# Kernel tuning notes

Hardware: AMD Instinct MI355X
Metric: run time of the kernel (lower is better)

Reference implementation:

```python
import jax, jax.numpy as jnp
import numpy as np
import math

B, T, C, H = 2, 2048, 768, 12
HD = C // H
EPS = 1e-5

def setup_inputs() -> dict:
    key = jax.random.key(0)
    ks = jax.random.split(key, 12)
    s = lambda n: 1.0 / math.sqrt(n)
    return {
        "x": jax.random.normal(ks[0], (B, T, C), jnp.float32),
        "ln1_g": jnp.ones((C,), jnp.float32),
        "ln1_b": jnp.zeros((C,), jnp.float32),
        "w_attn": jax.random.normal(ks[1], (C, 3 * C), jnp.float32) * s(C),
        "b_attn": jnp.zeros((3 * C,), jnp.float32),
        "w_proj": jax.random.normal(ks[2], (C, C), jnp.float32) * s(C),
        "b_proj": jnp.zeros((C,), jnp.float32),
        "ln2_g": jnp.ones((C,), jnp.float32),
        "ln2_b": jnp.zeros((C,), jnp.float32),
        "w_fc": jax.random.normal(ks[3], (C, 4 * C), jnp.float32) * s(C),
        "b_fc": jnp.zeros((4 * C,), jnp.float32),
        "w_fc2": jax.random.normal(ks[4], (4 * C, C), jnp.float32) * s(4 * C),
        "b_fc2": jnp.zeros((C,), jnp.float32),
    }

def layernorm(x, g, b):
    mu = jnp.mean(x, axis=-1, keepdims=True)
    var = jnp.mean(jnp.square(x - mu), axis=-1, keepdims=True)
    return (x - mu) * jax.lax.rsqrt(var + EPS) * g + b

def new_gelu(x):
    c = math.sqrt(2.0 / math.pi)
    return 0.5 * x * (1.0 + jnp.tanh(c * (x + 0.044715 * x ** 3)))

def reference(x, ln1_g, ln1_b, w_attn, b_attn, w_proj, b_proj,
              ln2_g, ln2_b, w_fc, b_fc, w_fc2, b_fc2):
    # --- attention branch ---
    h = layernorm(x, ln1_g, ln1_b)
    qkv = h @ w_attn + b_attn                       # [B,T,3C]
    q, k, v = jnp.split(qkv, 3, axis=-1)
    q = q.reshape(B, T, H, HD).transpose(0, 2, 1, 3)  # [B,H,T,hd]
    k = k.reshape(B, T, H, HD).transpose(0, 2, 1, 3)
    v = v.reshape(B, T, H, HD).transpose(0, 2, 1, 3)
    att = jnp.einsum('bhqd,bhkd->bhqk', q, k) * (1.0 / math.sqrt(HD))
    causal = jnp.tril(jnp.ones((T, T), bool))
    att = jnp.where(causal, att, -jnp.inf)
    att = jax.nn.softmax(att, axis=-1)
    y = jnp.einsum('bhqk,bhkd->bhqd', att, v)       # [B,H,T,hd]
    y = y.transpose(0, 2, 1, 3).reshape(B, T, C)
    x = x + y @ w_proj + b_proj
    # --- MLP branch ---
    h2 = layernorm(x, ln2_g, ln2_b)
    x = x + new_gelu(h2 @ w_fc + b_fc) @ w_fc2 + b_fc2
    return x
```

## Files before the change

### kernel.cpp

```cpp
#include <hip/hip_runtime.h>
#include <hip/hip_bf16.h>
#include <math.h>

typedef __hip_bfloat16 bf16;
typedef __attribute__((ext_vector_type(8))) short short8;
typedef __attribute__((ext_vector_type(4))) float floatx4;
typedef __attribute__((ext_vector_type(4))) unsigned uintx4;

#define GLDS16(g, l) __builtin_amdgcn_global_load_lds( \
    (const __attribute__((address_space(1))) void*)(g), \
    (__attribute__((address_space(3))) void*)(l), 16, 0, 0)

__device__ __forceinline__ bf16 f2bf(float v) { return __float2bfloat16(v); }

__device__ __forceinline__ unsigned cvtpk(float a, float b) {
  unsigned r;
  asm volatile("v_cvt_pk_bf16_f32 %0, %1, %2" : "=v"(r) : "v"(a), "v"(b));
  return r;
}

__global__ __launch_bounds__(256) void kconvT(const float* __restrict__ w,
                                              bf16* __restrict__ wT,
                                              int K, int N) {
  __shared__ float tile[32][33];
  const int n0 = blockIdx.x * 32, k0 = blockIdx.y * 32;
  const int tc = threadIdx.x & 31, tr = threadIdx.x >> 5;
#pragma unroll
  for (int p = 0; p < 4; p++)
    tile[tr + p * 8][tc] = w[(size_t)(k0 + tr + p * 8) * N + n0 + tc];
  __syncthreads();
#pragma unroll
  for (int p = 0; p < 4; p++)
    wT[(size_t)(n0 + tr + p * 8) * K + k0 + tc] = f2bf(tile[tc][tr + p * 8]);
}

__global__ __launch_bounds__(256) void kln(const float* __restrict__ x,
                                           const float* __restrict__ gw,
                                           const float* __restrict__ bw,
                                           bf16* __restrict__ out) {
  const int row = blockIdx.x, tid = threadIdx.x;
  const float* xr = x + (size_t)row * 768;
  float v0 = xr[tid], v1 = xr[tid + 256], v2 = xr[tid + 512];
  float s = v0 + v1 + v2;
  float s2 = v0 * v0 + v1 * v1 + v2 * v2;
#pragma unroll
  for (int off = 1; off < 64; off <<= 1) {
    s += __shfl_xor(s, off);
    s2 += __shfl_xor(s2, off);
  }
  __shared__ float red[8];
  const int wid = tid >> 6, lane = tid & 63;
  if (lane == 0) { red[wid] = s; red[4 + wid] = s2; }
  __syncthreads();
  s = red[0] + red[1] + red[2] + red[3];
  s2 = red[4] + red[5] + red[6] + red[7];
  const float mu = s * (1.f / 768.f);
  const float rst = rsqrtf(fmaxf(s2 * (1.f / 768.f) - mu * mu, 0.f) + 1e-5f);
  bf16* orow = out + (size_t)row * 768;
  orow[tid] = f2bf((v0 - mu) * rst * gw[tid] + bw[tid]);
  orow[tid + 256] = f2bf((v1 - mu) * rst * gw[tid + 256] + bw[tid + 256]);
  orow[tid + 512] = f2bf((v2 - mu) * rst * gw[tid + 512] + bw[tid + 512]);
}

__global__ __launch_bounds__(256) void kxpose(const bf16* __restrict__ qkv,
                                              bf16* __restrict__ VT) {
  const int T = 2048, C3 = 2304;
  const int t0 = blockIdx.x * 64, h = blockIdx.y, b = blockIdx.z;
  const int tid = threadIdx.x;
  __shared__ short tile[64][66];
  const bf16* src = qkv + (size_t)b * T * C3 + 1536 + h * 64;
  const int tr = tid >> 3, c = tid & 7;
#pragma unroll
  for (int p = 0; p < 2; p++) {
    short8 v = *(const short8*)(src + (size_t)(t0 + tr + p * 32) * C3 + c * 8);
    *(short8*)&tile[tr + p * 32][c * 8] = v;
  }
  __syncthreads();
  bf16* dst = VT + ((size_t)(b * 12 + h) * 64) * T + t0;
#pragma unroll
  for (int p = 0; p < 2; p++) {
    const int d = (tid >> 3) + p * 32, tc = tid & 7;
    short8 v;
#pragma unroll
    for (int j = 0; j < 8; j++) v[j] = tile[tc * 8 + j][d];
    *(short8*)(dst + (size_t)d * T + tc * 8) = v;
  }
}

template <int BN, int EPI>
__global__ __launch_bounds__(256, 2) void kgemm(
    const bf16* __restrict__ A, const bf16* __restrict__ BT,
    const float* __restrict__ bias, const float* __restrict__ resid,
    bf16* __restrict__ outb, float* __restrict__ outf, int M, int N, int K) {
  __shared__ bf16 As[2][128 * 32];
  __shared__ bf16 Bs[2][BN * 32];
  const int tid = threadIdx.x;
  const int wid = tid >> 6, lane = tid & 63, g = lane >> 4, q = lane & 15;
  constexpr int FM = (BN == 128) ? 4 : 2;
  constexpr int FN = 4;
  constexpr int WM = (BN == 128) ? 64 : 32;
  const int wr = (BN == 128) ? (wid >> 1) : wid;
  const int wc = (BN == 128) ? (wid & 1) : 0;
  const int row0 = blockIdx.y * 128, col0 = blockIdx.x * BN;
  floatx4 acc[FM][FN] = {};
  const int r0 = tid >> 2;
  const int c0 = (((tid & 3) ^ ((r0 >> 1) & 3))) * 8;
  const int lsl = (g ^ ((q >> 1) & 3)) * 16;
  const bf16* Ab = A + (size_t)row0 * K;
  const bf16* Bb = BT + (size_t)col0 * K;

  auto STAGE = [&](int kk, int buf) {
    GLDS16(Ab + (size_t)r0 * K + kk + c0, (char*)&As[buf][0] + wid * 1024);
    GLDS16(Ab + (size_t)(r0 + 64) * K + kk + c0,
           (char*)&As[buf][0] + 4096 + wid * 1024);
    GLDS16(Bb + (size_t)r0 * K + kk + c0, (char*)&Bs[buf][0] + wid * 1024);
    if constexpr (BN == 128)
      GLDS16(Bb + (size_t)(r0 + 64) * K + kk + c0,
             (char*)&Bs[buf][0] + 4096 + wid * 1024);
  };

  const int nk = K >> 5;
  STAGE(0, 0);
  asm volatile("s_waitcnt vmcnt(0)");
  __syncthreads();

  for (int kt = 0; kt < nk; kt++) {
    if (kt + 1 < nk) STAGE((kt + 1) << 5, (kt + 1) & 1);
    const char* Ac = (const char*)&As[kt & 1][0];
    const char* Bc = (const char*)&Bs[kt & 1][0];
    short8 af[FM], bfr[FN];
#pragma unroll
    for (int m = 0; m < FM; m++)
      af[m] = *(const short8*)(Ac + (wr * WM + m * 16 + q) * 64 + lsl);
#pragma unroll
    for (int n = 0; n < FN; n++)
      bfr[n] = *(const short8*)(Bc + (wc * 64 + n * 16 + q) * 64 + lsl);
#pragma unroll
    for (int m = 0; m < FM; m++)
#pragma unroll
      for (int n = 0; n < FN; n++)
        acc[m][n] =
            __builtin_amdgcn_mfma_f32_16x16x32_bf16(af[m], bfr[n], acc[m][n], 0, 0, 0);
    asm volatile("s_waitcnt vmcnt(0)");
    __syncthreads();
  }

#pragma unroll
  for (int n = 0; n < FN; n++) {
    const int col = col0 + wc * 64 + n * 16 + q;
    const float bv = bias[col];
#pragma unroll
    for (int m = 0; m < FM; m++) {
      const int rowb = row0 + wr * WM + m * 16 + g * 4;
#pragma unroll
      for (int r = 0; r < 4; r++) {
        const size_t idx = (size_t)(rowb + r) * N + col;
        const float v = acc[m][n][r] + bv;
        if (EPI == 0) {
          outb[idx] = f2bf(v);
        } else if (EPI == 1) {
          outf[idx] = v + resid[idx];
        } else {
          const float t = tanhf(0.7978845608028654f * (v + 0.044715f * v * v * v));
          outb[idx] = f2bf(0.5f * v * (1.0f + t));
        }
      }
    }
  }
}

__global__ __launch_bounds__(256, 2) void kattn(const bf16* __restrict__ qkv,
                                                const bf16* __restrict__ VT,
                                                bf16* __restrict__ y) {
  const int T = 2048, C3 = 2304;
  const int tid = threadIdx.x;
  const int w = tid >> 6, lane = tid & 63;
  const int g = lane >> 4, qi = lane & 15;

  const int bid = blockIdx.x;
  const int lb = (bid & 7) * 96 + (bid >> 3);
  const int qblk = 31 - (lb & 31);
  const int h = (lb >> 5) % 12, b = (lb >> 5) / 12;
  const int q0w = qblk * 64 + w * 16;
  const int qrow = q0w + qi;

  const bf16* Qb = qkv + (size_t)b * T * C3 + h * 64;
  const char* Ksrc = (const char*)(Qb + 768);
  const char* Vsrc = (const char*)(VT + (size_t)(b * 12 + h) * 64 * T);

  __shared__ __align__(16) char smem[32768];

  const int nt = qblk + 1;

  short8 qf[2];
#pragma unroll
  for (int s = 0; s < 2; s++)
    qf[s] = *(const short8*)(Qb + (size_t)qrow * C3 + s * 32 + g * 8);

  const int kvb = (qi >> 2) * 8 + (qi & 3);
  const unsigned swz = (unsigned)(((lane & 7) ^ (lane >> 3)) << 4);
  const int srow = lane >> 3;

  float m_run = -1e30f, l_run = 0.f;
  floatx4 o[4] = {};

#define STAGE(t)                                                                   \
  {                                                                                \
    char* base_ = smem + ((t) & 1) * 16384;                                        \
    const int kv0_ = (t) * 64;                                                     \
    _Pragma("unroll")                                                              \
    for (int j = 0; j < 2; j++) {                                                  \
      const int c_ = w * 2 + j;                                                    \
      GLDS16(Ksrc + (size_t)(kv0_ + c_ * 8 + srow) * 4608 + swz, base_ + c_ * 1024); \
      GLDS16(Vsrc + (size_t)(c_ * 8 + srow) * 4096 + kv0_ * 2 + swz,               \
             base_ + 8192 + c_ * 1024);                                            \
    }                                                                              \
  }

  STAGE(0);
  asm volatile("s_waitcnt vmcnt(0)");
  __syncthreads();

  for (int t = 0; t < nt; t++) {
    if (t + 1 < nt) STAGE(t + 1);
    const char* Kl = smem + (t & 1) * 16384;
    const char* Vl = Kl + 8192;
    const int kv0 = t * 64;

    short8 kf[8];
#pragma unroll
    for (int c = 0; c < 4; c++) {
      const int R = kvb + (c & 1) * 4 + (c >> 1) * 32;
#pragma unroll
      for (int s = 0; s < 2; s++)
        kf[c * 2 + s] =
            *(const short8*)(Kl + R * 128 + (((s * 4 + g) ^ (R & 7)) << 4));
    }
    short8 vfr[8];
#pragma unroll
    for (int ks = 0; ks < 2; ks++)
#pragma unroll
      for (int n = 0; n < 4; n++) {
        const int R2 = n * 16 + qi;
        vfr[ks * 4 + n] =
            *(const short8*)(Vl + R2 * 128 + (((ks * 4 + g) ^ (R2 & 7)) << 4));
      }

    floatx4 sacc[4] = {};
#pragma unroll
    for (int c = 0; c < 4; c++)
#pragma unroll
      for (int s = 0; s < 2; s++)
        sacc[c] =
            __builtin_amdgcn_mfma_f32_16x16x32_bf16(kf[c * 2 + s], qf[s], sacc[c], 0, 0, 0);

    if (kv0 + 63 > q0w) {
#pragma unroll
      for (int c = 0; c < 4; c++)
#pragma unroll
        for (int r = 0; r < 4; r++) {
          const int kv = kv0 + g * 8 + (c & 1) * 4 + r + (c >> 1) * 32;
          if (kv > qrow) sacc[c][r] = -1e30f;
        }
    }
    float mx = sacc[0][0];
#pragma unroll
    for (int c = 0; c < 4; c++)
#pragma unroll
      for (int r = 0; r < 4; r++) mx = fmaxf(mx, sacc[c][r]);
    mx = fmaxf(mx, __shfl_xor(mx, 16));
    mx = fmaxf(mx, __shfl_xor(mx, 32));
    mx *= 0.125f;
    const float mn = fmaxf(m_run, mx);
    const float al = __expf(m_run - mn);
    float ps = 0.f;
    unsigned pk[8];
#pragma unroll
    for (int c = 0; c < 4; c++) {
      float p0 = __expf(fmaf(sacc[c][0], 0.125f, -mn));
      float p1 = __expf(fmaf(sacc[c][1], 0.125f, -mn));
      float p2 = __expf(fmaf(sacc[c][2], 0.125f, -mn));
      float p3 = __expf(fmaf(sacc[c][3], 0.125f, -mn));
      ps += (p0 + p1) + (p2 + p3);
      pk[c * 2] = cvtpk(p0, p1);
      pk[c * 2 + 1] = cvtpk(p2, p3);
    }
    ps += __shfl_xor(ps, 16);
    ps += __shfl_xor(ps, 32);
    l_run = l_run * al + ps;
    m_run = mn;
#pragma unroll
    for (int n = 0; n < 4; n++) o[n] *= al;

#pragma unroll
    for (int ks = 0; ks < 2; ks++) {
      uintx4 pu;
      pu.x = pk[ks * 4 + 0];
      pu.y = pk[ks * 4 + 1];
      pu.z = pk[ks * 4 + 2];
      pu.w = pk[ks * 4 + 3];
      const short8 pf = __builtin_bit_cast(short8, pu);
#pragma unroll
      for (int n = 0; n < 4; n++)
        o[n] = __builtin_amdgcn_mfma_f32_16x16x32_bf16(vfr[ks * 4 + n], pf, o[n], 0, 0, 0);
    }

    asm volatile("s_waitcnt vmcnt(0)");
    __syncthreads();
  }
#undef STAGE

  const float inv = 1.0f / l_run;
  bf16* yr = y + (size_t)(b * T + qrow) * 768 + h * 64;
#pragma unroll
  for (int n = 0; n < 4; n++) {
    uint2 pr;
    pr.x = cvtpk(o[n][0] * inv, o[n][1] * inv);
    pr.y = cvtpk(o[n][2] * inv, o[n][3] * inv);
    *(uint2*)(yr + n * 16 + g * 4) = pr;
  }
}

extern "C" void kernel_launch(void* const* d_in, const int* in_sizes, int n_in,
                              void* d_out, int out_size, void* d_ws, size_t ws_size,
                              hipStream_t stream) {
  const float* x      = (const float*)d_in[0];
  const float* ln1_g  = (const float*)d_in[1];
  const float* ln1_b  = (const float*)d_in[2];
  const float* w_attn = (const float*)d_in[3];
  const float* b_attn = (const float*)d_in[4];
  const float* w_proj = (const float*)d_in[5];
  const float* b_proj = (const float*)d_in[6];
  const float* ln2_g  = (const float*)d_in[7];
  const float* ln2_b  = (const float*)d_in[8];
  const float* w_fc   = (const float*)d_in[9];
  const float* b_fc   = (const float*)d_in[10];
  const float* w_fc2  = (const float*)d_in[11];
  const float* b_fc2  = (const float*)d_in[12];
  float* out = (float*)d_out;

  const int M = 4096;
  char* p = (char*)d_ws;
  bf16* wT_attn = (bf16*)p; p += (size_t)2304 * 768 * 2;
  bf16* wT_proj = (bf16*)p; p += (size_t)768 * 768 * 2;
  bf16* wT_fc   = (bf16*)p; p += (size_t)3072 * 768 * 2;
  bf16* wT_fc2  = (bf16*)p; p += (size_t)768 * 3072 * 2;
  bf16* h       = (bf16*)p; p += (size_t)M * 768 * 2;
  bf16* qkv     = (bf16*)p;
  bf16* yb      = (bf16*)(p + (size_t)M * 2304 * 2);
  bf16* act     = qkv;      p += (size_t)M * 2304 * 2 + (size_t)M * 768 * 2;
  float* x1     = (float*)p;
  bf16* VT      = (bf16*)p;

  kconvT<<<dim3(2304 / 32, 768 / 32), 256, 0, stream>>>(w_attn, wT_attn, 768, 2304);
  kconvT<<<dim3(768 / 32, 768 / 32), 256, 0, stream>>>(w_proj, wT_proj, 768, 768);
  kconvT<<<dim3(3072 / 32, 768 / 32), 256, 0, stream>>>(w_fc, wT_fc, 768, 3072);
  kconvT<<<dim3(768 / 32, 3072 / 32), 256, 0, stream>>>(w_fc2, wT_fc2, 3072, 768);

  kln<<<M, 256, 0, stream>>>(x, ln1_g, ln1_b, h);
  kgemm<128, 0><<<dim3(2304 / 128, M / 128), 256, 0, stream>>>(
      h, wT_attn, b_attn, nullptr, qkv, nullptr, M, 2304, 768);
  kxpose<<<dim3(32, 12, 2), 256, 0, stream>>>(qkv, VT);
  kattn<<<dim3(768), 256, 0, stream>>>(qkv, VT, yb);
  kgemm<64, 1><<<dim3(768 / 64, M / 128), 256, 0, stream>>>(
      yb, wT_proj, b_proj, x, nullptr, x1, M, 768, 768);

  kln<<<M, 256, 0, stream>>>(x1, ln2_g, ln2_b, h);
  kgemm<128, 2><<<dim3(3072 / 128, M / 128), 256, 0, stream>>>(
      h, wT_fc, b_fc, nullptr, act, nullptr, M, 3072, 768);
  kgemm<64, 1><<<dim3(768 / 64, M / 128), 256, 0, stream>>>(
      act, wT_fc2, b_fc2, x1, nullptr, out, M, 768, 3072);
}
```

Before: 212.9 us.

## Triple-buffer GEMM LDS pipeline and remap blocks for XCD-aware scheduling

The GEMM kernel moves from a double-buffered to a triple-buffered LDS pipeline that prefetches two K-tiles ahead. Partial vmcnt waits replace the full drain, so global-to-LDS loads overlap more MFMA work. The grid is flattened to 1D and block IDs are remapped so that consecutive logical tiles land on the same XCD (bid&7 striding), which is meant to improve L2 reuse of A and B tiles. The extra LDS buffer raises shared memory use per block, which could reduce occupancy.

```diff
diff --git a/kernel.cpp b/kernel.cpp
--- a/kernel.cpp
+++ b/kernel.cpp
@@ -91,9 +91,10 @@
 __global__ __launch_bounds__(256, 2) void kgemm(
     const bf16* __restrict__ A, const bf16* __restrict__ BT,
     const float* __restrict__ bias, const float* __restrict__ resid,
-    bf16* __restrict__ outb, float* __restrict__ outf, int M, int N, int K) {
-  __shared__ bf16 As[2][128 * 32];
-  __shared__ bf16 Bs[2][BN * 32];
+    bf16* __restrict__ outb, float* __restrict__ outf, int M, int N, int K,
+    int NXB) {
+  __shared__ bf16 As[3][128 * 32];
+  __shared__ bf16 Bs[3][BN * 32];
   const int tid = threadIdx.x;
   const int wid = tid >> 6, lane = tid & 63, g = lane >> 4, q = lane & 15;
   constexpr int FM = (BN == 128) ? 4 : 2;
@@ -101,7 +102,11 @@
   constexpr int WM = (BN == 128) ? 64 : 32;
   const int wr = (BN == 128) ? (wid >> 1) : wid;
   const int wc = (BN == 128) ? (wid & 1) : 0;
-  const int row0 = blockIdx.y * 128, col0 = blockIdx.x * BN;
+
+  const int bid = blockIdx.x;
+  const int lb = (bid & 7) * ((int)gridDim.x >> 3) + (bid >> 3);
+  const int row0 = (lb / NXB) * 128, col0 = (lb % NXB) * BN;
+
   floatx4 acc[FM][FN] = {};
   const int r0 = tid >> 2;
   const int c0 = (((tid & 3) ^ ((r0 >> 1) & 3))) * 8;
@@ -121,13 +126,23 @@
 
   const int nk = K >> 5;
   STAGE(0, 0);
-  asm volatile("s_waitcnt vmcnt(0)");
-  __syncthreads();
+  STAGE(32, 1);
 
   for (int kt = 0; kt < nk; kt++) {
-    if (kt + 1 < nk) STAGE((kt + 1) << 5, (kt + 1) & 1);
-    const char* Ac = (const char*)&As[kt & 1][0];
-    const char* Bc = (const char*)&Bs[kt & 1][0];
+    if (kt + 2 < nk) {
+      STAGE((kt + 2) << 5, (kt + 2) % 3);
+      if constexpr (BN == 128) asm volatile("s_waitcnt vmcnt(8)");
+      else asm volatile("s_waitcnt vmcnt(6)");
+    } else if (kt + 1 < nk) {
+      if constexpr (BN == 128) asm volatile("s_waitcnt vmcnt(4)");
+      else asm volatile("s_waitcnt vmcnt(3)");
+    } else {
+      asm volatile("s_waitcnt vmcnt(0)");
+    }
+    __syncthreads();
+
+    const char* Ac = (const char*)&As[kt % 3][0];
+    const char* Bc = (const char*)&Bs[kt % 3][0];
     short8 af[FM], bfr[FN];
 #pragma unroll
     for (int m = 0; m < FM; m++)
@@ -141,7 +156,6 @@
       for (int n = 0; n < FN; n++)
         acc[m][n] =
             __builtin_amdgcn_mfma_f32_16x16x32_bf16(af[m], bfr[n], acc[m][n], 0, 0, 0);
-    asm volatile("s_waitcnt vmcnt(0)");
     __syncthreads();
   }
 
@@ -358,16 +372,16 @@
   kconvT<<<dim3(768 / 32, 3072 / 32), 256, 0, stream>>>(w_fc2, wT_fc2, 3072, 768);
 
   kln<<<M, 256, 0, stream>>>(x, ln1_g, ln1_b, h);
-  kgemm<128, 0><<<dim3(2304 / 128, M / 128), 256, 0, stream>>>(
-      h, wT_attn, b_attn, nullptr, qkv, nullptr, M, 2304, 768);
+  kgemm<128, 0><<<dim3(18 * 32), 256, 0, stream>>>(
+      h, wT_attn, b_attn, nullptr, qkv, nullptr, M, 2304, 768, 18);
   kxpose<<<dim3(32, 12, 2), 256, 0, stream>>>(qkv, VT);
   kattn<<<dim3(768), 256, 0, stream>>>(qkv, VT, yb);
-  kgemm<64, 1><<<dim3(768 / 64, M / 128), 256, 0, stream>>>(
-      yb, wT_proj, b_proj, x, nullptr, x1, M, 768, 768);
+  kgemm<64, 1><<<dim3(12 * 32), 256, 0, stream>>>(
+      yb, wT_proj, b_proj, x, nullptr, x1, M, 768, 768, 12);
 
   kln<<<M, 256, 0, stream>>>(x1, ln2_g, ln2_b, h);
-  kgemm<128, 2><<<dim3(3072 / 128, M / 128), 256, 0, stream>>>(
-      h, wT_fc, b_fc, nullptr, act, nullptr, M, 3072, 768);
-  kgemm<64, 1><<<dim3(768 / 64, M / 128), 256, 0, stream>>>(
-      act, wT_fc2, b_fc2, x1, nullptr, out, M, 768, 3072);
-}
+  kgemm<128, 2><<<dim3(24 * 32), 256, 0, stream>>>(
+      h, wT_fc, b_fc, nullptr, act, nullptr, M, 3072, 768, 24);
+  kgemm<64, 1><<<dim3(12 * 32), 256, 0, stream>>>(
+      act, wT_fc2, b_fc2, x1, nullptr, out, M, 768, 3072, 12);
+}
```

Result: no change. 211.1 us (-0.9%).
